# Kernel tuning notes

Measured on AMD Instinct MI355X. Metric: run time of the kernel, lower is better.

The kernel has to match this reference:

```python
import jax, jax.numpy as jnp
import numpy as np

B, L, D0, H, K = 16, 256, 64, 128, 512  # batch, seq, feat, hidden, codebook size


def _p(key, shape, scale=0.05):
    return jax.random.normal(key, shape, jnp.float32) * scale


def setup_inputs() -> dict:
    key = jax.random.key(0)
    ks = jax.random.split(key, 32)
    inp = {
        "inputs": jax.random.normal(ks[0], (B, L, D0), jnp.float32),
        "input_lens": jnp.full((B,), L, dtype=jnp.int64),
        "in_mask": jnp.ones((B, L), jnp.float32),
        # encoder params
        "enc_lin1_W": _p(ks[1], (H, D0)), "enc_lin1_b": jnp.zeros((H,), jnp.float32),
        "enc_Wih_f": _p(ks[2], (4 * H, H)), "enc_Whh_f": _p(ks[3], (4 * H, H)), "enc_b_f": jnp.zeros((4 * H,), jnp.float32),
        "enc_Wih_b": _p(ks[4], (4 * H, H)), "enc_Whh_b": _p(ks[5], (4 * H, H)), "enc_b_b": jnp.zeros((4 * H,), jnp.float32),
        "enc_lin2_W": _p(ks[6], (H, 2 * H)), "enc_lin2_b": jnp.zeros((H,), jnp.float32),
        # VQ codebook (K codes of dim H), init uniform(-1/K, 1/K) as in torch
        "vq_emb": jax.random.uniform(ks[7], (K, H), jnp.float32, -1.0 / K, 1.0 / K),
        # decoder params
        "dec_lin1_W": _p(ks[8], (H, D0)), "dec_lin1_b": jnp.zeros((H,), jnp.float32),
        "dec_Wih": _p(ks[9], (4 * H, H)), "dec_Whh": _p(ks[10], (4 * H, H)), "dec_b": jnp.zeros((4 * H,), jnp.float32),
        "attn_Wq": _p(ks[11], (H, H)), "attn_bq": jnp.zeros((H,), jnp.float32),
        "attn_Wk": _p(ks[12], (H, H)), "attn_bk": jnp.zeros((H,), jnp.float32),
        "attn_Wv": _p(ks[13], (H, H)), "attn_bv": jnp.zeros((H,), jnp.float32),
        "dec_lin2_W": _p(ks[14], (D0, H)), "dec_lin2_b": jnp.zeros((D0,), jnp.float32),
    }
    return inp


def _lstm_cell(x, h, c, Wih, Whh, b):
    g = x @ Wih.T + h @ Whh.T + b  # (B, 4H)
    i, f, gg, o = jnp.split(g, 4, axis=-1)
    c = jax.nn.sigmoid(f) * c + jax.nn.sigmoid(i) * jnp.tanh(gg)
    h = jax.nn.sigmoid(o) * jnp.tanh(c)
    return h, c


def _lstm_scan(x_blh, Wih, Whh, b, reverse=False):
    Bb = x_blh.shape[0]
    Hh = Whh.shape[1]
    init = (jnp.zeros((Bb, Hh), x_blh.dtype), jnp.zeros((Bb, Hh), x_blh.dtype))

    def step(carry, x):
        h, c = _lstm_cell(x, carry[0], carry[1], Wih, Whh, b)
        return (h, c), h

    _, hs = jax.lax.scan(step, init, jnp.swapaxes(x_blh, 0, 1), reverse=reverse)
    return jnp.swapaxes(hs, 0, 1)  # (B, L, H)


def _forward(inputs, in_mask, p):
    # ---- encoder: Linear -> ReLU -> BiLSTM -> Linear (full-length sequences) ----
    enc_x = jax.nn.relu(inputs @ p["enc_lin1_W"].T + p["enc_lin1_b"])
    hf = _lstm_scan(enc_x, p["enc_Wih_f"], p["enc_Whh_f"], p["enc_b_f"], reverse=False)
    hb = _lstm_scan(enc_x, p["enc_Wih_b"], p["enc_Whh_b"], p["enc_b_b"], reverse=True)
    ze = jnp.concatenate([hf, hb], axis=-1) @ p["enc_lin2_W"].T + p["enc_lin2_b"]  # (B,L,H)

    # ---- VQ: nearest codebook entry (expanded ||a-b||^2, avoids (B,L,K,C) tensor) ----
    emb = p["vq_emb"]  # (K, H)
    dist = (jnp.sum(ze * ze, -1, keepdims=True)
            - 2.0 * jnp.einsum("blc,kc->blk", ze, emb)
            + jnp.sum(emb * emb, -1)[None, None, :])  # (B,L,K)
    nearest = jnp.argmin(dist, axis=-1)  # (B,L) int
    zq = emb[nearest]  # (B,L,H)
    dec_in = ze + jax.lax.stop_gradient(zq - ze)  # straight-through

    k_proj = dec_in @ p["attn_Wk"].T + p["attn_bk"]  # (B,L,H)
    v_proj = dec_in @ p["attn_Wv"].T + p["attn_bv"]
    scale = 1.0 / jnp.sqrt(jnp.float32(H))
    mask_add = jnp.where(in_mask == 0, -1e9, 0.0).astype(jnp.float32)  # (B,L)

    def dec_step(carry, _):
        h, c, tok = carry
        x = jax.nn.relu(tok @ p["dec_lin1_W"].T + p["dec_lin1_b"])  # (B,H)
        h, c = _lstm_cell(x, h, c, p["dec_Wih"], p["dec_Whh"], p["dec_b"])
        q = h @ p["attn_Wq"].T + p["attn_bq"]  # (B,H)
        scores = jnp.einsum("bd,bld->bl", q, k_proj) * scale + mask_add
        attn = jax.nn.softmax(scores, axis=-1)  # (B,L)
        ctx = jnp.einsum("bl,bld->bd", attn, v_proj)  # (B,H)
        out = ctx @ p["dec_lin2_W"].T + p["dec_lin2_b"]  # (B,D0)
        return (h, c, out), (out, attn)

    Bb = inputs.shape[0]
    init = (jnp.zeros((Bb, H), jnp.float32), jnp.zeros((Bb, H), jnp.float32), jnp.zeros((Bb, D0), jnp.float32))
    _, (outs, attns) = jax.lax.scan(dec_step, init, None, length=dec_in.shape[1])
    dec_out = jnp.swapaxes(outs, 0, 1)  # (B,L,D0)
    attn_w = jnp.swapaxes(attns, 0, 1)  # (B,L,L)
    return dec_out, attn_w, ze, zq


def reference(inputs, input_lens, in_mask, enc_lin1_W, enc_lin1_b, enc_Wih_f, enc_Whh_f, enc_b_f,
              enc_Wih_b, enc_Whh_b, enc_b_b, enc_lin2_W, enc_lin2_b, vq_emb,
              dec_lin1_W, dec_lin1_b, dec_Wih, dec_Whh, dec_b,
              attn_Wq, attn_bq, attn_Wk, attn_bk, attn_Wv, attn_bv, dec_lin2_W, dec_lin2_b):
    p = dict(enc_lin1_W=enc_lin1_W, enc_lin1_b=enc_lin1_b, enc_Wih_f=enc_Wih_f, enc_Whh_f=enc_Whh_f,
             enc_b_f=enc_b_f, enc_Wih_b=enc_Wih_b, enc_Whh_b=enc_Whh_b, enc_b_b=enc_b_b,
             enc_lin2_W=enc_lin2_W, enc_lin2_b=enc_lin2_b, vq_emb=vq_emb,
             dec_lin1_W=dec_lin1_W, dec_lin1_b=dec_lin1_b, dec_Wih=dec_Wih, dec_Whh=dec_Whh, dec_b=dec_b,
             attn_Wq=attn_Wq, attn_bq=attn_bq, attn_Wk=attn_Wk, attn_bk=attn_bk,
             attn_Wv=attn_Wv, attn_bv=attn_bv, dec_lin2_W=dec_lin2_W, dec_lin2_b=dec_lin2_b)
    return _forward(inputs, in_mask, p)
```

## Files before the change

### kernel.cpp

```cpp
#include <hip/hip_runtime.h>

#define Bn  16
#define Ln  256
#define D0n 64
#define Hn  128
#define H4n 512
#define Kn  512
#define BLn 4096

typedef float f4 __attribute__((ext_vector_type(4)));
typedef unsigned long long u64;

__device__ __forceinline__ float sigf(float x) { return 1.0f / (1.0f + expf(-x)); }

__device__ __forceinline__ float fma4v(f4 w, f4 x, float acc) {
    acc = fmaf(w.x, x.x, acc);
    acc = fmaf(w.y, x.y, acc);
    acc = fmaf(w.z, x.z, acc);
    acc = fmaf(w.w, x.w, acc);
    return acc;
}

__device__ __forceinline__ float dotn(const f4* __restrict__ a,
                                      const f4* __restrict__ w, int n4) {
    float a0 = 0.f, a1 = 0.f, a2 = 0.f, a3 = 0.f;
    for (int i = 0; i < n4; i += 4) {
        a0 = fma4v(a[i], w[i], a0);
        a1 = fma4v(a[i + 1], w[i + 1], a1);
        a2 = fma4v(a[i + 2], w[i + 2], a2);
        a3 = fma4v(a[i + 3], w[i + 3], a3);
    }
    return (a0 + a1) + (a2 + a3);
}

__device__ __forceinline__ void tag_store(u64* p, float v, unsigned tag) {
    u64 pk = ((u64)tag << 32) | (u64)__float_as_uint(v);
    __hip_atomic_store(p, pk, __ATOMIC_RELAXED, __HIP_MEMORY_SCOPE_AGENT);
}
__device__ __forceinline__ float tag_poll(u64* p, unsigned tag) {
    u64 v;
    do {
        v = __hip_atomic_load(p, __ATOMIC_RELAXED, __HIP_MEMORY_SCOPE_AGENT);
    } while ((unsigned)(v >> 32) != tag);
    return __uint_as_float((unsigned)v);
}

__global__ __launch_bounds__(256)
void k_gemm(const float* __restrict__ X, const float* __restrict__ W,
            const float* __restrict__ b, float* __restrict__ Y,
            int K, int out_dim, int do_relu, float scale) {
    __shared__ f4 wt[4160];
    const int K4 = K >> 2;
    const int st = K4 + 1;
    const int lg = __ffs(K4) - 1;
    const int tid = threadIdx.x;
    const int c = tid & 63, rpart = tid >> 6;
    const f4* W4 = (const f4*)W;
    const int per = (64 * K4) >> 8;
    for (int i = 0; i < per; ++i) {
        int idx = i * 256 + tid;
        int row = idx >> lg, col = idx & (K4 - 1);
        wt[row * st + col] = W4[(size_t)(blockIdx.x * 64 + row) * K4 + col];
    }
    __syncthreads();
    const f4* X4 = (const f4*)X;
    const float bc = b ? b[blockIdx.x * 64 + c] : 0.f;
    const f4* wrow = wt + c * st;
    for (int i = 0; i < 16; ++i) {
        int r = blockIdx.y * 64 + i * 4 + rpart;
        const f4* xr = X4 + (size_t)r * K4;
        float a0 = 0.f, a1 = 0.f, a2 = 0.f, a3 = 0.f;
        for (int k = 0; k < K4; k += 4) {
            a0 = fma4v(wrow[k],     xr[k],     a0);
            a1 = fma4v(wrow[k + 1], xr[k + 1], a1);
            a2 = fma4v(wrow[k + 2], xr[k + 2], a2);
            a3 = fma4v(wrow[k + 3], xr[k + 3], a3);
        }
        float acc = scale * ((a0 + a1) + (a2 + a3)) + bc;
        if (do_relu) acc = fmaxf(acc, 0.f);
        Y[(size_t)r * out_dim + blockIdx.x * 64 + c] = acc;
    }
}

__global__ void k_transpose(const float* __restrict__ in, float* __restrict__ out,
                            int R, int C) {
    int idx = blockIdx.x * blockDim.x + threadIdx.x;
    if (idx >= R * C) return;
    int c = idx / R, r = idx % R;
    out[idx] = in[(size_t)r * C + c];
}

__global__ void k_zero(int* __restrict__ p, int n) {
    int i = blockIdx.x * blockDim.x + threadIdx.x;
    if (i < n) p[i] = 0;
}

__global__ void k_rearrWihBC(const f4* __restrict__ in, f4* __restrict__ out) {
    int idx = blockIdx.x * blockDim.x + threadIdx.x;
    if (idx >= 16384) return;
    int tid = idx & 511, k = (idx >> 9) & 15, side = idx >> 13;
    int w = tid >> 6, lane = tid & 63;
    int q = lane >> 4, j2 = (lane & 15) >> 1, half = lane & 1;
    int grow = q * 128 + side * 64 + w * 8 + j2;
    out[idx] = in[(size_t)grow * 32 + half * 16 + k];
}

__global__ void k_rearrWhhL(const f4* __restrict__ whf, const f4* __restrict__ whb,
                            f4* __restrict__ out) {
    int idx = blockIdx.x * blockDim.x + threadIdx.x;
    if (idx >= 16384) return;
    int row = idx & 511, k = (idx >> 9) & 15, dir = idx >> 13;
    const f4* src = dir ? whb : whf;
    out[idx] = src[(size_t)row * 32 + 16 + k];
}

__global__ void k_rearrKQF(const f4* __restrict__ in, f4* __restrict__ out) {
    int idx = blockIdx.x * blockDim.x + threadIdx.x;
    if (idx >= 131072) return;
    int tid = idx & 511, k = (idx >> 9) & 15, b = idx >> 13;
    out[idx] = in[((size_t)b * 256 + (tid >> 1)) * 32 + (tid & 1) * 16 + k];
}

__global__ void k_cst(const float* __restrict__ kp, const float* __restrict__ bq,
                      const float* __restrict__ mask, float* __restrict__ cst) {
    int p = blockIdx.x * blockDim.x + threadIdx.x;
    if (p >= BLn) return;
    float a = dotn((const f4*)bq, (const f4*)(kp + (size_t)p * Hn), Hn >> 2);
    cst[p] = a * 0.088388347648318447f + (mask[p] == 0.f ? -1e9f : 0.f);
}

__global__ void k_codenorm(const float* __restrict__ emb, float* __restrict__ c2) {
    int k = blockIdx.x * blockDim.x + threadIdx.x;
    if (k >= Kn) return;
    const f4* e4 = (const f4*)(emb + (size_t)k * Hn);
    float acc = 0.f;
    for (int i = 0; i < Hn / 4; ++i) {
        f4 v = e4[i];
        acc = fmaf(v.x, v.x, acc); acc = fmaf(v.y, v.y, acc);
        acc = fmaf(v.z, v.z, acc); acc = fmaf(v.w, v.w, acc);
    }
    c2[k] = acc;
}

__global__ __launch_bounds__(128)
void k_vqpick(const float* __restrict__ dist, const float* __restrict__ emb,
              float* __restrict__ zq) {
    const int p = blockIdx.x, tid = threadIdx.x;
    __shared__ int best_s;
    if (tid < 64) {
        float best = 3.0e38f; int bi = 0;
        for (int j = 0; j < 8; ++j) {
            int k = j * 64 + tid;
            float d = dist[(size_t)p * Kn + k];
            if (d < best) { best = d; bi = k; }
        }
        for (int off = 32; off > 0; off >>= 1) {
            float ov = __shfl_xor(best, off);
            int   oi = __shfl_xor(bi, off);
            if (ov < best || (ov == best && oi < bi)) { best = ov; bi = oi; }
        }
        if (tid == 0) best_s = bi;
    }
    __syncthreads();
    zq[(size_t)p * Hn + tid] = emb[(size_t)best_s * Hn + tid];
}

__global__ __launch_bounds__(512, 1)
void k_lstm3(const float* __restrict__ xWf, const float* __restrict__ xWb,
             const float* __restrict__ Whh_f, const float* __restrict__ Whh_b,
             const float* __restrict__ WhhL_g, float* __restrict__ hcat) {
    const int b   = blockIdx.x & 15;
    const int dir = blockIdx.x >> 4;
    const int tid = threadIdx.x;
    const float* xW  = dir ? xWb : xWf;
    const f4* Whh4   = (const f4*)(dir ? Whh_b : Whh_f);

    __shared__ __align__(16) f4 wh2_s[16 * 512];
    __shared__ __align__(16) float h_s[Hn];
    __shared__ float g_s[H4n];

    f4 w[16];
#pragma unroll
    for (int f = 0; f < 16; ++f) w[f] = Whh4[(size_t)tid * 32 + f];
#pragma unroll
    for (int f = 0; f < 16; ++f) asm volatile("" : "+v"(w[f]));

    const f4* WhhL4 = (const f4*)WhhL_g;
#pragma unroll
    for (int k = 0; k < 16; ++k)
        wh2_s[k * 512 + tid] = WhhL4[(size_t)dir * 8192 + k * 512 + tid];

    float c_reg = 0.f;
    if (tid < Hn) h_s[tid] = 0.f;

    const int t0 = dir ? (Ln - 1) : 0;
    float xw_v = xW[((size_t)b * Ln + t0) * H4n + tid];
    __syncthreads();

    for (int s = 0; s < Ln; ++s) {
        const int t = dir ? (Ln - 1 - s) : s;
        float xw_n = 0.f;
        if (s + 1 < Ln) {
            int tn = dir ? (Ln - 2 - s) : (s + 1);
            xw_n = xW[((size_t)b * Ln + tn) * H4n + tid];
        }
        {
            const f4* h4 = (const f4*)h_s;
            float a0 = 0.f, a1 = 0.f, a2 = 0.f, a3 = 0.f;
#pragma unroll
            for (int f = 0; f < 16; f += 4) {
                a0 = fma4v(w[f],     h4[f],     a0);
                a1 = fma4v(w[f + 1], h4[f + 1], a1);
                a2 = fma4v(w[f + 2], h4[f + 2], a2);
                a3 = fma4v(w[f + 3], h4[f + 3], a3);
            }
#pragma unroll
            for (int f = 0; f < 16; f += 4) {
                a0 = fma4v(wh2_s[f * 512 + tid],       h4[16 + f],     a0);
                a1 = fma4v(wh2_s[(f + 1) * 512 + tid], h4[16 + f + 1], a1);
                a2 = fma4v(wh2_s[(f + 2) * 512 + tid], h4[16 + f + 2], a2);
                a3 = fma4v(wh2_s[(f + 3) * 512 + tid], h4[16 + f + 3], a3);
            }
            g_s[tid] = (a0 + a1) + (a2 + a3) + xw_v;
        }
        __syncthreads();
        if (tid < Hn) {
            float ig = sigf(g_s[tid]);
            float fg = sigf(g_s[Hn + tid]);
            float gg = tanhf(g_s[2 * Hn + tid]);
            float og = sigf(g_s[3 * Hn + tid]);
            c_reg = fg * c_reg + ig * gg;
            float hv = og * tanhf(c_reg);
            h_s[tid] = hv;
            hcat[((size_t)b * Ln + t) * (2 * Hn) + dir * Hn + tid] = hv;
        }
        __syncthreads();
        xw_v = xw_n;
    }
}

__global__ __launch_bounds__(512, 1)
void k_decoder(const float* __restrict__ kqF_g, const float* __restrict__ vw_g,
               const float* __restrict__ cst_g,
               const float* __restrict__ W1,  const float* __restrict__ b1_g,
               const float* __restrict__ WihBC_g, const float* __restrict__ Whh,
               const float* __restrict__ bd_g, u64* gxd,
               float* __restrict__ dec_out, float* __restrict__ attn_w) {
    const int b    = blockIdx.x & 15;
    const int side = blockIdx.x >> 4;
    const int tid  = threadIdx.x;

    __shared__ __align__(16) f4 wih_s[16 * 512];
    __shared__ __align__(16) float tok_s[D0n];
    __shared__ __align__(16) float x_s[Hn];
    __shared__ __align__(16) float h_s[Hn];
    __shared__ float s_s[Ln];
    __shared__ float attn_sp[8][33];
    __shared__ float cst_s[Ln];
    __shared__ float b1_s[Hn];

    const int w    = tid >> 6;
    const int lane = tid & 63;
    const int q    = lane >> 4;
    const int j2   = (lane & 15) >> 1;
    const int half = lane & 1;
    const int grow = q * 128 + side * 64 + w * 8 + j2;

    const f4* Whh4 = (const f4*)Whh;
    f4 whh[16];
#pragma unroll
    for (int f = 0; f < 16; ++f) whh[f] = Whh4[(size_t)grow * 32 + half * 16 + f];
    float bdr = bd_g[grow];
    const int o = tid >> 3, slab = tid & 7;
    float vwr[32];
#pragma unroll
    for (int l = 0; l < 32; ++l)
        vwr[l] = vw_g[((size_t)b * Ln + slab * 32 + l) * D0n + o];
#pragma unroll
    for (int f = 0; f < 16; ++f) asm volatile("" : "+v"(whh[f]));
#pragma unroll
    for (int l = 0; l < 32; ++l) asm volatile("" : "+v"(vwr[l]));
    asm volatile("" : "+v"(bdr));

    const f4* WihBC4 = (const f4*)WihBC_g;
#pragma unroll
    for (int k = 0; k < 16; ++k)
        wih_s[k * 512 + tid] = WihBC4[(size_t)side * 8192 + k * 512 + tid];
    if (tid < D0n) tok_s[tid] = 0.f;
    if (tid < Hn)  { h_s[tid] = 0.f; b1_s[tid] = b1_g[tid]; }
    if (tid < Ln)  cst_s[tid] = cst_g[(size_t)b * Ln + tid];
    float c_reg = 0.f;
    __syncthreads();

    u64* gx_mine = gxd + (b * 2 + side) * 128;
    u64* gx_peer = gxd + (b * 2 + (side ^ 1)) * 128;

    const int ar = tid >> 2, ap = tid & 3;
    const f4* W1_4 = (const f4*)W1;
    const f4* kqF  = (const f4*)kqF_g + (size_t)b * 8192;
    const int dbase = (tid & 1) * 16;

    for (int t = 0; t < Ln; ++t) {
        {
            const f4* t4 = (const f4*)tok_s;
            float u0 = 0.f, u1 = 0.f;
#pragma unroll
            for (int k = 0; k < 4; k += 2) {
                f4 wa  = W1_4[(size_t)ar * 16 + ap * 4 + k];
                f4 wb2 = W1_4[(size_t)ar * 16 + ap * 4 + k + 1];
                u0 = fma4v(wa,  t4[ap * 4 + k],     u0);
                u1 = fma4v(wb2, t4[ap * 4 + k + 1], u1);
            }
            float a = u0 + u1;
            a += __shfl_xor(a, 1);
            a += __shfl_xor(a, 2);
            if (ap == 0) x_s[ar] = fmaxf(a + b1_s[ar], 0.f);
        }
        __syncthreads();
        {
            const f4* x4 = (const f4*)x_s + half * 16;
            const f4* h4 = (const f4*)h_s + half * 16;
            float a0 = 0.f, a1 = 0.f, a2 = 0.f, a3 = 0.f;
#pragma unroll
            for (int f = 0; f < 16; f += 4) {
                a0 = fma4v(wih_s[f * 512 + tid],       x4[f],     a0);
                a1 = fma4v(wih_s[(f + 1) * 512 + tid], x4[f + 1], a1);
                a2 = fma4v(wih_s[(f + 2) * 512 + tid], x4[f + 2], a2);
                a3 = fma4v(wih_s[(f + 3) * 512 + tid], x4[f + 3], a3);
            }
#pragma unroll
            for (int f = 0; f < 16; f += 4) {
                a0 = fma4v(whh[f],     h4[f],     a0);
                a1 = fma4v(whh[f + 1], h4[f + 1], a1);
                a2 = fma4v(whh[f + 2], h4[f + 2], a2);
                a3 = fma4v(whh[f + 3], h4[f + 3], a3);
            }
            float g = (a0 + a1) + (a2 + a3);
            g += __shfl_xor(g, 1);
            g += bdr;
            float gI = __shfl(g, (lane & 15));
            float gF = __shfl(g, (lane & 15) + 16);
            float gG = __shfl(g, (lane & 15) + 32);
            float gO = __shfl(g, (lane & 15) + 48);
            if (lane < 16 && half == 0) {
                float ig = sigf(gI), fg = sigf(gF);
                float gg = tanhf(gG), og = sigf(gO);
                c_reg = fg * c_reg + ig * gg;
                float hv = og * tanhf(c_reg);
                int idx = w * 8 + j2;
                h_s[side * 64 + idx] = hv;
                tag_store(&gx_mine[(t & 1) * 64 + idx], hv, (unsigned)(t + 1));
            }
            if (lane < 16 && half == 1) {
                int idx = w * 8 + j2;
                h_s[(side ^ 1) * 64 + idx] =
                    tag_poll(&gx_peer[(t & 1) * 64 + idx], (unsigned)(t + 1));
            }
        }
        __syncthreads();
        {
            const f4* h4 = (const f4*)h_s;
            float a0 = 0.f, a1 = 0.f;
#pragma unroll
            for (int k = 0; k < 16; k += 2) {
                f4 q0 = kqF[(size_t)k * 512 + tid];
                f4 q1 = kqF[(size_t)(k + 1) * 512 + tid];
                a0 = fma4v(q0, h4[dbase + k],     a0);
                a1 = fma4v(q1, h4[dbase + k + 1], a1);
            }
            float a = a0 + a1;
            a += __shfl_xor(a, 1);
            if ((tid & 1) == 0) s_s[tid >> 1] = a + cst_s[tid >> 1];
        }
        __syncthreads();
        if (tid < 64) {
            float v0 = s_s[tid],       v1 = s_s[tid + 64];
            float v2 = s_s[tid + 128], v3 = s_s[tid + 192];
            float m = fmaxf(fmaxf(v0, v1), fmaxf(v2, v3));
#pragma unroll
            for (int o2 = 32; o2 > 0; o2 >>= 1) m = fmaxf(m, __shfl_xor(m, o2));
            float e0 = expf(v0 - m), e1 = expf(v1 - m);
            float e2 = expf(v2 - m), e3 = expf(v3 - m);
            float ss = (e0 + e1) + (e2 + e3);
#pragma unroll
            for (int o2 = 32; o2 > 0; o2 >>= 1) ss += __shfl_xor(ss, o2);
            float inv = 1.f / ss;
            e0 *= inv; e1 *= inv; e2 *= inv; e3 *= inv;
            attn_sp[tid >> 5][tid & 31] = e0;
            attn_sp[(tid + 64) >> 5][tid & 31] = e1;
            attn_sp[(tid + 128) >> 5][tid & 31] = e2;
            attn_sp[(tid + 192) >> 5][tid & 31] = e3;
            if (side == 0) {
                float* aw = attn_w + ((size_t)b * Ln + t) * Ln;
                aw[tid] = e0; aw[tid + 64] = e1;
                aw[tid + 128] = e2; aw[tid + 192] = e3;
            }
        }
        __syncthreads();
        {
            const float* as = attn_sp[slab];
            float g0 = 0.f, g1 = 0.f, g2 = 0.f, g3 = 0.f;
#pragma unroll
            for (int l = 0; l < 32; l += 4) {
                g0 = fmaf(as[l],     vwr[l],     g0);
                g1 = fmaf(as[l + 1], vwr[l + 1], g1);
                g2 = fmaf(as[l + 2], vwr[l + 2], g2);
                g3 = fmaf(as[l + 3], vwr[l + 3], g3);
            }
            float a = (g0 + g1) + (g2 + g3);
            a += __shfl_xor(a, 1);
            a += __shfl_xor(a, 2);
            a += __shfl_xor(a, 4);
            if (slab == 0) {
                tok_s[o] = a;
                if (side == 1) dec_out[((size_t)b * Ln + t) * D0n + o] = a;
            }
        }
        __syncthreads();
    }
}

extern "C" void kernel_launch(void* const* d_in, const int* in_sizes, int n_in,
                              void* d_out, int out_size, void* d_ws, size_t ws_size,
                              hipStream_t stream) {
    const float* inputs     = (const float*)d_in[0];
    const float* in_mask    = (const float*)d_in[2];
    const float* enc_lin1_W = (const float*)d_in[3];
    const float* enc_lin1_b = (const float*)d_in[4];
    const float* enc_Wih_f  = (const float*)d_in[5];
    const float* enc_Whh_f  = (const float*)d_in[6];
    const float* enc_b_f    = (const float*)d_in[7];
    const float* enc_Wih_b  = (const float*)d_in[8];
    const float* enc_Whh_b  = (const float*)d_in[9];
    const float* enc_b_b    = (const float*)d_in[10];
    const float* enc_lin2_W = (const float*)d_in[11];
    const float* enc_lin2_b = (const float*)d_in[12];
    const float* vq_emb     = (const float*)d_in[13];
    const float* dec_lin1_W = (const float*)d_in[14];
    const float* dec_lin1_b = (const float*)d_in[15];
    const float* dec_Wih    = (const float*)d_in[16];
    const float* dec_Whh    = (const float*)d_in[17];
    const float* dec_b      = (const float*)d_in[18];
    const float* attn_Wq    = (const float*)d_in[19];
    const float* attn_bq    = (const float*)d_in[20];
    const float* attn_Wk    = (const float*)d_in[21];
    const float* attn_bk    = (const float*)d_in[22];
    const float* attn_Wv    = (const float*)d_in[23];
    const float* attn_bv    = (const float*)d_in[24];
    const float* dec_lin2_W = (const float*)d_in[25];
    const float* dec_lin2_b = (const float*)d_in[26];

    float* out     = (float*)d_out;
    float* dec_out = out;
    float* attn_w  = out + 262144;
    float* ze      = out + 1310720;
    float* zq      = out + 1835008;

    float* ws    = (float*)d_ws;
    float* enc_x = ws;
    float* xWf   = enc_x + 524288;
    float* xWb   = xWf + 2097152;
    float* hcat  = xWb + 2097152;
    float* kp    = hcat + 1048576;
    float* vp    = kp + 524288;
    float* c2    = vp + 524288;
    u64*   gxd   = (u64*)(c2 + 512);
    float* WqT   = enc_x;
    float* WihBC = enc_x + 16384;
    float* WhhL  = enc_x + 16384 + 65536;
    float* dist  = xWf;
    float* KQF   = xWf;
    float* kq    = xWb;
    float* vw    = xWb + 524288;
    float* cst   = xWb + 786432;

    dim3 blk(256);
    k_gemm<<<dim3(2, 64), blk, 0, stream>>>(inputs, enc_lin1_W, enc_lin1_b, enc_x, D0n, Hn, 1, 1.f);
    k_gemm<<<dim3(8, 64), blk, 0, stream>>>(enc_x, enc_Wih_f, enc_b_f, xWf, Hn, H4n, 0, 1.f);
    k_gemm<<<dim3(8, 64), blk, 0, stream>>>(enc_x, enc_Wih_b, enc_b_b, xWb, Hn, H4n, 0, 1.f);
    k_transpose<<<64, 256, 0, stream>>>(attn_Wq, WqT, Hn, Hn);
    k_rearrWihBC<<<64, 256, 0, stream>>>((const f4*)dec_Wih, (f4*)WihBC);
    k_rearrWhhL<<<64, 256, 0, stream>>>((const f4*)enc_Whh_f, (const f4*)enc_Whh_b, (f4*)WhhL);
    k_zero<<<32, 256, 0, stream>>>((int*)gxd, 8192);
    k_lstm3<<<32, 512, 0, stream>>>(xWf, xWb, enc_Whh_f, enc_Whh_b, WhhL, hcat);
    k_gemm<<<dim3(2, 64), blk, 0, stream>>>(hcat, enc_lin2_W, enc_lin2_b, ze, 2 * Hn, Hn, 0, 1.f);
    k_codenorm<<<2, 256, 0, stream>>>(vq_emb, c2);
    k_gemm<<<dim3(8, 64), blk, 0, stream>>>(ze, vq_emb, c2, dist, Hn, Kn, 0, -2.f);
    k_vqpick<<<BLn, 128, 0, stream>>>(dist, vq_emb, zq);
    k_gemm<<<dim3(2, 64), blk, 0, stream>>>(zq, attn_Wk, attn_bk, kp, Hn, Hn, 0, 1.f);
    k_gemm<<<dim3(2, 64), blk, 0, stream>>>(zq, attn_Wv, attn_bv, vp, Hn, Hn, 0, 1.f);
    k_gemm<<<dim3(2, 64), blk, 0, stream>>>(kp, WqT, nullptr, kq, Hn, Hn, 0, 0.088388347648318447f);
    k_rearrKQF<<<512, 256, 0, stream>>>((const f4*)kq, (f4*)KQF);
    k_gemm<<<dim3(1, 64), blk, 0, stream>>>(vp, dec_lin2_W, dec_lin2_b, vw, Hn, D0n, 0, 1.f);
    k_cst<<<Bn, 256, 0, stream>>>(kp, attn_bq, in_mask, cst);
    k_decoder<<<32, 512, 0, stream>>>(KQF, vw, cst,
                                      dec_lin1_W, dec_lin1_b,
                                      WihBC, dec_Whh, dec_b, gxd,
                                      dec_out, attn_w);
}
```

Baseline: 1.687 ms.

## Restructure decoder gate reduction and softmax, merge prep kernels into one launch

Merges the four small preprocessing kernels (Wq transpose, Wih rearrange, Whh rearrange, zeroing) into one k_prep launch to cut launch overhead. In the decoder, gate rows now map to threads so each row's gate sum goes to shared memory, and 64 threads apply the LSTM cell instead of the earlier shuffle-based gather. The softmax is computed redundantly by every wavefront into per-wave attention buffers, so a block-wide barrier is replaced by a wave-local s_waitcnt. This adds one barrier in the gate stage and repeats the softmax work in all eight waves.

```diff
diff --git a/kernel.cpp b/kernel.cpp
--- a/kernel.cpp
+++ b/kernel.cpp
@@ -82,36 +82,30 @@
     }
 }
 
-__global__ void k_transpose(const float* __restrict__ in, float* __restrict__ out,
-                            int R, int C) {
-    int idx = blockIdx.x * blockDim.x + threadIdx.x;
-    if (idx >= R * C) return;
-    int c = idx / R, r = idx % R;
-    out[idx] = in[(size_t)r * C + c];
-}
-
-__global__ void k_zero(int* __restrict__ p, int n) {
-    int i = blockIdx.x * blockDim.x + threadIdx.x;
-    if (i < n) p[i] = 0;
-}
-
-__global__ void k_rearrWihBC(const f4* __restrict__ in, f4* __restrict__ out) {
-    int idx = blockIdx.x * blockDim.x + threadIdx.x;
-    if (idx >= 16384) return;
-    int tid = idx & 511, k = (idx >> 9) & 15, side = idx >> 13;
-    int w = tid >> 6, lane = tid & 63;
-    int q = lane >> 4, j2 = (lane & 15) >> 1, half = lane & 1;
-    int grow = q * 128 + side * 64 + w * 8 + j2;
-    out[idx] = in[(size_t)grow * 32 + half * 16 + k];
-}
-
-__global__ void k_rearrWhhL(const f4* __restrict__ whf, const f4* __restrict__ whb,
-                            f4* __restrict__ out) {
-    int idx = blockIdx.x * blockDim.x + threadIdx.x;
-    if (idx >= 16384) return;
-    int row = idx & 511, k = (idx >> 9) & 15, dir = idx >> 13;
-    const f4* src = dir ? whb : whf;
-    out[idx] = src[(size_t)row * 32 + 16 + k];
+__global__ void k_prep(const float* __restrict__ attn_Wq, float* __restrict__ WqT,
+                       const f4* __restrict__ dec_Wih, f4* __restrict__ WihL,
+                       const f4* __restrict__ whf, const f4* __restrict__ whb,
+                       f4* __restrict__ WhhL, int* __restrict__ zbuf) {
+    const int blk = blockIdx.x, tid = threadIdx.x;
+    if (blk < 64) {
+        int idx = blk * 256 + tid;
+        int c = idx >> 7, r = idx & 127;
+        WqT[idx] = attn_Wq[(size_t)r * Hn + c];
+    } else if (blk < 128) {
+        int idx = (blk - 64) * 256 + tid;
+        int t = idx & 511, side = (idx >> 9) & 1, k = idx >> 10;
+        int rl = t >> 1;
+        int grow = (rl >> 6) * 128 + side * 64 + (rl & 63);
+        WihL[idx] = dec_Wih[(size_t)grow * 32 + (t & 1) * 16 + k];
+    } else if (blk < 192) {
+        int idx = (blk - 128) * 256 + tid;
+        int row = idx & 511, k = (idx >> 9) & 15, dir = idx >> 13;
+        const f4* src = dir ? whb : whf;
+        WhhL[idx] = src[(size_t)row * 32 + 16 + k];
+    } else {
+        int idx = (blk - 192) * 256 + tid;
+        if (idx < 8192) zbuf[idx] = 0;
+    }
 }
 
 __global__ void k_rearrKQF(const f4* __restrict__ in, f4* __restrict__ out) {
@@ -243,7 +237,7 @@
 void k_decoder(const float* __restrict__ kqF_g, const float* __restrict__ vw_g,
                const float* __restrict__ cst_g,
                const float* __restrict__ W1,  const float* __restrict__ b1_g,
-               const float* __restrict__ WihBC_g, const float* __restrict__ Whh,
+               const float* __restrict__ WihL_g, const float* __restrict__ Whh,
                const float* __restrict__ bd_g, u64* gxd,
                float* __restrict__ dec_out, float* __restrict__ attn_w) {
     const int b    = blockIdx.x & 15;
@@ -254,22 +248,19 @@
     __shared__ __align__(16) float tok_s[D0n];
     __shared__ __align__(16) float x_s[Hn];
     __shared__ __align__(16) float h_s[Hn];
+    __shared__ float g_loc[256];
     __shared__ float s_s[Ln];
-    __shared__ float attn_sp[8][33];
+    __shared__ float attn8[8][8][33];
     __shared__ float cst_s[Ln];
     __shared__ float b1_s[Hn];
 
-    const int w    = tid >> 6;
-    const int lane = tid & 63;
-    const int q    = lane >> 4;
-    const int j2   = (lane & 15) >> 1;
-    const int half = lane & 1;
-    const int grow = q * 128 + side * 64 + w * 8 + j2;
+    const int rl = tid >> 1, ghalf = tid & 1;
+    const int grow = (rl >> 6) * 128 + side * 64 + (rl & 63);
 
     const f4* Whh4 = (const f4*)Whh;
     f4 whh[16];
 #pragma unroll
-    for (int f = 0; f < 16; ++f) whh[f] = Whh4[(size_t)grow * 32 + half * 16 + f];
+    for (int f = 0; f < 16; ++f) whh[f] = Whh4[(size_t)grow * 32 + ghalf * 16 + f];
     float bdr = bd_g[grow];
     const int o = tid >> 3, slab = tid & 7;
     float vwr[32];
@@ -282,10 +273,10 @@
     for (int l = 0; l < 32; ++l) asm volatile("" : "+v"(vwr[l]));
     asm volatile("" : "+v"(bdr));
 
-    const f4* WihBC4 = (const f4*)WihBC_g;
+    const f4* WihL4 = (const f4*)WihL_g;
 #pragma unroll
     for (int k = 0; k < 16; ++k)
-        wih_s[k * 512 + tid] = WihBC4[(size_t)side * 8192 + k * 512 + tid];
+        wih_s[k * 512 + tid] = WihL4[(size_t)k * 1024 + side * 512 + tid];
     if (tid < D0n) tok_s[tid] = 0.f;
     if (tid < Hn)  { h_s[tid] = 0.f; b1_s[tid] = b1_g[tid]; }
     if (tid < Ln)  cst_s[tid] = cst_g[(size_t)b * Ln + tid];
@@ -299,6 +290,7 @@
     const f4* W1_4 = (const f4*)W1;
     const f4* kqF  = (const f4*)kqF_g + (size_t)b * 8192;
     const int dbase = (tid & 1) * 16;
+    const int wv = tid >> 6, lane = tid & 63;
 
     for (int t = 0; t < Ln; ++t) {
         {
@@ -318,8 +310,8 @@
         }
         __syncthreads();
         {
-            const f4* x4 = (const f4*)x_s + half * 16;
-            const f4* h4 = (const f4*)h_s + half * 16;
+            const f4* x4 = (const f4*)x_s + ghalf * 16;
+            const f4* h4 = (const f4*)h_s + ghalf * 16;
             float a0 = 0.f, a1 = 0.f, a2 = 0.f, a3 = 0.f;
 #pragma unroll
             for (int f = 0; f < 16; f += 4) {
@@ -335,27 +327,22 @@
                 a2 = fma4v(whh[f + 2], h4[f + 2], a2);
                 a3 = fma4v(whh[f + 3], h4[f + 3], a3);
             }
-            float g = (a0 + a1) + (a2 + a3);
-            g += __shfl_xor(g, 1);
-            g += bdr;
-            float gI = __shfl(g, (lane & 15));
-            float gF = __shfl(g, (lane & 15) + 16);
-            float gG = __shfl(g, (lane & 15) + 32);
-            float gO = __shfl(g, (lane & 15) + 48);
-            if (lane < 16 && half == 0) {
-                float ig = sigf(gI), fg = sigf(gF);
-                float gg = tanhf(gG), og = sigf(gO);
-                c_reg = fg * c_reg + ig * gg;
-                float hv = og * tanhf(c_reg);
-                int idx = w * 8 + j2;
-                h_s[side * 64 + idx] = hv;
-                tag_store(&gx_mine[(t & 1) * 64 + idx], hv, (unsigned)(t + 1));
-            }
-            if (lane < 16 && half == 1) {
-                int idx = w * 8 + j2;
-                h_s[(side ^ 1) * 64 + idx] =
-                    tag_poll(&gx_peer[(t & 1) * 64 + idx], (unsigned)(t + 1));
-            }
+            float a = (a0 + a1) + (a2 + a3);
+            a += __shfl_xor(a, 1);
+            if (ghalf == 0) g_loc[rl] = a + bdr;
+        }
+        __syncthreads();
+        if (tid < 64) {
+            float ig = sigf(g_loc[tid]);
+            float fg = sigf(g_loc[64 + tid]);
+            float gg = tanhf(g_loc[128 + tid]);
+            float og = sigf(g_loc[192 + tid]);
+            c_reg = fg * c_reg + ig * gg;
+            float hv = og * tanhf(c_reg);
+            h_s[side * 64 + tid] = hv;
+            tag_store(&gx_mine[(t & 1) * 64 + tid], hv, (unsigned)(t + 1));
+            h_s[(side ^ 1) * 64 + tid] =
+                tag_poll(&gx_peer[(t & 1) * 64 + tid], (unsigned)(t + 1));
         }
         __syncthreads();
         {
@@ -373,9 +360,9 @@
             if ((tid & 1) == 0) s_s[tid >> 1] = a + cst_s[tid >> 1];
         }
         __syncthreads();
-        if (tid < 64) {
-            float v0 = s_s[tid],       v1 = s_s[tid + 64];
-            float v2 = s_s[tid + 128], v3 = s_s[tid + 192];
+        {
+            float v0 = s_s[lane],       v1 = s_s[lane + 64];
+            float v2 = s_s[lane + 128], v3 = s_s[lane + 192];
             float m = fmaxf(fmaxf(v0, v1), fmaxf(v2, v3));
 #pragma unroll
             for (int o2 = 32; o2 > 0; o2 >>= 1) m = fmaxf(m, __shfl_xor(m, o2));
@@ -386,19 +373,17 @@
             for (int o2 = 32; o2 > 0; o2 >>= 1) ss += __shfl_xor(ss, o2);
             float inv = 1.f / ss;
             e0 *= inv; e1 *= inv; e2 *= inv; e3 *= inv;
-            attn_sp[tid >> 5][tid & 31] = e0;
-            attn_sp[(tid + 64) >> 5][tid & 31] = e1;
-            attn_sp[(tid + 128) >> 5][tid & 31] = e2;
-            attn_sp[(tid + 192) >> 5][tid & 31] = e3;
-            if (side == 0) {
+            attn8[wv][lane >> 5][lane & 31] = e0;
+            attn8[wv][(lane + 64) >> 5][lane & 31] = e1;
+            attn8[wv][(lane + 128) >> 5][lane & 31] = e2;
+            attn8[wv][(lane + 192) >> 5][lane & 31] = e3;
+            if (side == 0 && wv == 0) {
                 float* aw = attn_w + ((size_t)b * Ln + t) * Ln;
-                aw[tid] = e0; aw[tid + 64] = e1;
-                aw[tid + 128] = e2; aw[tid + 192] = e3;
-            }
-        }
-        __syncthreads();
-        {
-            const float* as = attn_sp[slab];
+                aw[lane] = e0; aw[lane + 64] = e1;
+                aw[lane + 128] = e2; aw[lane + 192] = e3;
+            }
+            asm volatile("s_waitcnt lgkmcnt(0)" ::: "memory");
+            const float* as = attn8[wv][slab];
             float g0 = 0.f, g1 = 0.f, g2 = 0.f, g3 = 0.f;
 #pragma unroll
             for (int l = 0; l < 32; l += 4) {
@@ -466,7 +451,7 @@
     float* c2    = vp + 524288;
     u64*   gxd   = (u64*)(c2 + 512);
     float* WqT   = enc_x;
-    float* WihBC = enc_x + 16384;
+    float* WihL  = enc_x + 16384;
     float* WhhL  = enc_x + 16384 + 65536;
     float* dist  = xWf;
     float* KQF   = xWf;
@@ -478,10 +463,9 @@
     k_gemm<<<dim3(2, 64), blk, 0, stream>>>(inputs, enc_lin1_W, enc_lin1_b, enc_x, D0n, Hn, 1, 1.f);
     k_gemm<<<dim3(8, 64), blk, 0, stream>>>(enc_x, enc_Wih_f, enc_b_f, xWf, Hn, H4n, 0, 1.f);
     k_gemm<<<dim3(8, 64), blk, 0, stream>>>(enc_x, enc_Wih_b, enc_b_b, xWb, Hn, H4n, 0, 1.f);
-    k_transpose<<<64, 256, 0, stream>>>(attn_Wq, WqT, Hn, Hn);
-    k_rearrWihBC<<<64, 256, 0, stream>>>((const f4*)dec_Wih, (f4*)WihBC);
-    k_rearrWhhL<<<64, 256, 0, stream>>>((const f4*)enc_Whh_f, (const f4*)enc_Whh_b, (f4*)WhhL);
-    k_zero<<<32, 256, 0, stream>>>((int*)gxd, 8192);
+    k_prep<<<224, 256, 0, stream>>>(attn_Wq, WqT, (const f4*)dec_Wih, (f4*)WihL,
+                                    (const f4*)enc_Whh_f, (const f4*)enc_Whh_b,
+                                    (f4*)WhhL, (int*)gxd);
     k_lstm3<<<32, 512, 0, stream>>>(xWf, xWb, enc_Whh_f, enc_Whh_b, WhhL, hcat);
     k_gemm<<<dim3(2, 64), blk, 0, stream>>>(hcat, enc_lin2_W, enc_lin2_b, ze, 2 * Hn, Hn, 0, 1.f);
     k_codenorm<<<2, 256, 0, stream>>>(vq_emb, c2);
@@ -495,6 +479,6 @@
     k_cst<<<Bn, 256, 0, stream>>>(kp, attn_bq, in_mask, cst);
     k_decoder<<<32, 512, 0, stream>>>(KQF, vw, cst,
                                       dec_lin1_W, dec_lin1_b,
-                                      WihBC, dec_Whh, dec_b, gxd,
+                                      WihL, dec_Whh, dec_b, gxd,
                                       dec_out, attn_w);
 }
```

Result: faster. 1.633 ms (-3.2%).
